# Kernel tuning notes

Hardware: AMD Instinct MI355X
Metric: run time of the kernel (lower is better)

## Reference

```python
import jax, jax.numpy as jnp
import numpy as np

B, S, L, F, CD, NH, E, HID = 4, 1024, 256, 512, 768, 8, 8, 2048


def _xavier(k, shape):
    std = float(np.sqrt(1.0 / (shape[-2] + shape[-1])))
    return jax.random.normal(k, shape, dtype=jnp.float32) * std


def setup_inputs() -> dict:
    key = jax.random.key(0)
    ks = iter(jax.random.split(key, 64))
    nk = lambda: next(ks)
    inp = {}
    inp['x_r'] = jax.random.normal(nk(), (B, S, F), jnp.float32)
    inp['x_i'] = jax.random.normal(nk(), (B, S, F), jnp.float32)
    inp['ctx_r'] = jax.random.normal(nk(), (B, L, CD), jnp.float32)
    inp['ctx_i'] = jax.random.normal(nk(), (B, L, CD), jnp.float32)
    inp['ln1_g'] = jnp.ones((F,), jnp.float32)
    inp['ln2_g'] = jnp.ones((F,), jnp.float32)
    inp['ln3_g'] = jnp.ones((F,), jnp.float32)
    for pref, shp in [('sa_q', (F, F)), ('sa_k', (F, F)), ('sa_v', (F, F)), ('sa_o', (F, F)),
                      ('ca_q', (F, F)), ('ca_k', (CD, F)), ('ca_v', (CD, F)), ('ca_o', (F, F))]:
        inp[pref + 'Wr'] = _xavier(nk(), shp)
        inp[pref + 'Wi'] = _xavier(nk(), shp)
        inp[pref + 'br'] = jnp.zeros((F,), jnp.float32)
        inp[pref + 'bi'] = jnp.zeros((F,), jnp.float32)
    inp['moe_W1r'] = _xavier(nk(), (E, F, HID))
    inp['moe_W1i'] = _xavier(nk(), (E, F, HID))
    inp['moe_b1r'] = jnp.zeros((E, HID), jnp.float32)
    inp['moe_b1i'] = jnp.zeros((E, HID), jnp.float32)
    inp['moe_mb'] = jnp.zeros((E, HID), jnp.float32)  # modReLU bias
    inp['moe_W2r'] = _xavier(nk(), (E, HID, F))
    inp['moe_W2i'] = _xavier(nk(), (E, HID, F))
    inp['moe_b2r'] = jnp.zeros((E, F), jnp.float32)
    inp['moe_b2i'] = jnp.zeros((E, F), jnp.float32)
    return inp


def _clin(xr, xi, Wr, Wi, br, bi):
    # (xr + i xi) @ (Wr + i Wi) + (br + i bi)
    return xr @ Wr - xi @ Wi + br, xr @ Wi + xi @ Wr + bi


def _cln(xr, xi, g, eps=1e-6):
    amp = jnp.sqrt(xr * xr + xi * xi + eps)
    s = g * (amp / (jnp.mean(amp, axis=-1, keepdims=True) + eps)) / (amp + eps)
    return xr * s, xi * s


def _modrelu(xr, xi, b, eps=1e-10):
    amp = jnp.sqrt(xr * xr + xi * xi + eps)
    s = jax.nn.relu(amp + b) / (amp + eps)
    return xr * s, xi * s


def _cattn(xr, xi, cr, ci, qWr, qWi, qbr, qbi, kWr, kWi, kbr, kbi,
           vWr, vWi, vbr, vbi, oWr, oWi, obr, obi, nh):
    qr, qi = _clin(xr, xi, qWr, qWi, qbr, qbi)
    kr, ki = _clin(cr, ci, kWr, kWi, kbr, kbi)
    vr, vi = _clin(cr, ci, vWr, vWi, vbr, vbi)
    Bt, Sq, Ft = qr.shape
    Sk = kr.shape[1]
    d = Ft // nh
    sp = lambda t: t.reshape(Bt, t.shape[1], nh, d).transpose(0, 2, 1, 3)  # b n s d
    Qr, Qi, Kr, Ki, Vr, Vi = sp(qr), sp(qi), sp(kr), sp(ki), sp(vr), sp(vi)
    scale = 1.0 / float(d) ** 0.5
    scores = (jnp.einsum('bnqd,bnkd->bnqk', Qr, Kr)
              + jnp.einsum('bnqd,bnkd->bnqk', Qi, Ki)) * scale
    w = jax.nn.softmax(scores, axis=-1)
    mix = lambda t: jnp.einsum('bnqk,bnkd->bnqd', w, t).transpose(0, 2, 1, 3).reshape(Bt, Sq, Ft)
    return _clin(mix(Vr), mix(Vi), oWr, oWi, obr, obi)


def reference(x_r, x_i, ctx_r, ctx_i, ln1_g, ln2_g, ln3_g,
              sa_qWr, sa_qWi, sa_qbr, sa_qbi, sa_kWr, sa_kWi, sa_kbr, sa_kbi,
              sa_vWr, sa_vWi, sa_vbr, sa_vbi, sa_oWr, sa_oWi, sa_obr, sa_obi,
              ca_qWr, ca_qWi, ca_qbr, ca_qbi, ca_kWr, ca_kWi, ca_kbr, ca_kbi,
              ca_vWr, ca_vWi, ca_vbr, ca_vbi, ca_oWr, ca_oWi, ca_obr, ca_obi,
              moe_W1r, moe_W1i, moe_b1r, moe_b1i, moe_mb,
              moe_W2r, moe_W2i, moe_b2r, moe_b2i):
    # self-attention block
    hr, hi = _cln(x_r, x_i, ln1_g)
    ar, ai = _cattn(hr, hi, hr, hi, sa_qWr, sa_qWi, sa_qbr, sa_qbi,
                    sa_kWr, sa_kWi, sa_kbr, sa_kbi, sa_vWr, sa_vWi, sa_vbr, sa_vbi,
                    sa_oWr, sa_oWi, sa_obr, sa_obi, NH)
    xr, xi = x_r + ar, x_i + ai
    # cross-attention block
    hr, hi = _cln(xr, xi, ln2_g)
    ar, ai = _cattn(hr, hi, ctx_r, ctx_i, ca_qWr, ca_qWi, ca_qbr, ca_qbi,
                    ca_kWr, ca_kWi, ca_kbr, ca_kbi, ca_vWr, ca_vWi, ca_vbr, ca_vbi,
                    ca_oWr, ca_oWi, ca_obr, ca_obi, NH)
    xr, xi = xr + ar, xi + ai
    # phase-routed MoE block
    hr, hi = _cln(xr, xi, ln3_g)
    phase = jnp.arctan2(hi, hr)
    token_phase = jnp.arctan2(jnp.mean(jnp.sin(phase), axis=-1),
                              jnp.mean(jnp.cos(phase), axis=-1))
    idx = jnp.clip(jnp.floor((token_phase + jnp.pi) / (2.0 * jnp.pi) * E).astype(jnp.int32), 0, E - 1)
    acc_r = jnp.zeros_like(hr)
    acc_i = jnp.zeros_like(hi)
    for e in range(E):  # dense-compute-then-mask, faithful to source
        ur, ui = _clin(hr, hi, moe_W1r[e], moe_W1i[e], moe_b1r[e], moe_b1i[e])
        ur, ui = _modrelu(ur, ui, moe_mb[e])
        yr, yi = _clin(ur, ui, moe_W2r[e], moe_W2i[e], moe_b2r[e], moe_b2i[e])
        m = (idx == e).astype(hr.dtype)[..., None]
        acc_r = acc_r + yr * m
        acc_i = acc_i + yi * m
    xr, xi = xr + acc_r, xi + acc_i
    return jnp.stack([xr, xi])  # [2, B, S, F] real/imag
```

## Files before the change

### kernel.cpp

```cpp
#include <hip/hip_runtime.h>
#include <hip/hip_bf16.h>
#include <math.h>


#define NTOK 4096
#define FF   512
#define CDIM 768
#define NEXP 8
#define HID  2048
#define TMAX 72
#define NPAD (TMAX * 64)

typedef __hip_bfloat16 bf16;
typedef short bf16x8 __attribute__((ext_vector_type(8)));
typedef float f32x4  __attribute__((ext_vector_type(4)));

struct Ptr6 { const float* p[6]; };

__device__ __forceinline__ short f2bf(float x) {
    unsigned u = __float_as_uint(x);
    unsigned r = (u + 0x7fff + ((u >> 16) & 1)) >> 16;
    return (short)r;
}
__device__ __forceinline__ float bf2f(short s) {
    return __uint_as_float(((unsigned)(unsigned short)s) << 16);
}
__device__ __forceinline__ void gload16(const void* g, void* l) {
    __builtin_amdgcn_global_load_lds(
        (const __attribute__((address_space(1))) unsigned int*)g,
        (__attribute__((address_space(3))) unsigned int*)l, 16, 0, 0);
}

__global__ __launch_bounds__(256)
void cln_kernel(const float* __restrict__ xr, const float* __restrict__ xi,
                const float* __restrict__ g,
                float* __restrict__ hr, float* __restrict__ hi)
{
    const int F = FF;
    long base = (long)blockIdx.x * F;
    int t = threadIdx.x;
    int j0 = t, j1 = t + 256;
    float xr0 = xr[base + j0], xi0 = xi[base + j0];
    float xr1 = xr[base + j1], xi1 = xi[base + j1];
    float a0 = sqrtf(xr0 * xr0 + xi0 * xi0 + 1e-6f);
    float a1 = sqrtf(xr1 * xr1 + xi1 * xi1 + 1e-6f);
    float s = a0 + a1;
#pragma unroll
    for (int off = 32; off >= 1; off >>= 1) s += __shfl_xor(s, off);
    __shared__ float wsum[4];
    if ((t & 63) == 0) wsum[t >> 6] = s;
    __syncthreads();
    float mean = (wsum[0] + wsum[1] + wsum[2] + wsum[3]) * (1.0f / 512.0f);
    float d0 = g[j0] * (a0 / (mean + 1e-6f)) / (a0 + 1e-6f);
    float d1 = g[j1] * (a1 / (mean + 1e-6f)) / (a1 + 1e-6f);
    hr[base + j0] = xr0 * d0;  hi[base + j0] = xi0 * d0;
    hr[base + j1] = xr1 * d1;  hi[base + j1] = xi1 * d1;
}

__global__ __launch_bounds__(256)
void expandA_x2(const float* __restrict__ sR, const float* __restrict__ sI,
                bf16* __restrict__ dR, bf16* __restrict__ dI, int K)
{
    int k = blockIdx.x * 256 + threadIdx.x;
    int m = blockIdx.y;
    long s = (long)m * K + k;
    long d = (long)m * 2 * K + k;
    float a = sR[s];
    bf16 ah = __float2bfloat16(a);
    dR[d] = ah; dR[d + K] = __float2bfloat16(a - __bfloat162float(ah));
    float b = sI[s];
    bf16 bh = __float2bfloat16(b);
    dI[d] = bh; dI[d + K] = __float2bfloat16(b - __bfloat162float(bh));
}

__global__ __launch_bounds__(256)
void convA_plain(const float* __restrict__ sR, const float* __restrict__ sI,
                 bf16* __restrict__ dR, bf16* __restrict__ dI, int K)
{
    int k = blockIdx.x * 256 + threadIdx.x;
    long s = (long)blockIdx.y * K + k;
    dR[s] = __float2bfloat16(sR[s]);
    dI[s] = __float2bfloat16(sI[s]);
}

__global__ __launch_bounds__(256)
void expandW_x2_packed(const float* __restrict__ sR, const float* __restrict__ sI,
                       bf16* __restrict__ dR, bf16* __restrict__ dI,
                       int N, int kdiv)
{
    int g = blockIdx.x * 256 + threadIdx.x;
    int nt = g >> 6, l = g & 63;
    int kc = blockIdx.y;
    int lo = (kc >= kdiv);
    int kb = (kc - (lo ? kdiv : 0)) * 32 + (l >> 4) * 8;
    int n  = nt * 16 + (l & 15);
    long dbase = ((long)kc * (N >> 4) + nt) * 512 + l * 8;
#pragma unroll
    for (int j = 0; j < 8; j++) {
        float a = sR[(long)(kb + j) * N + n];
        bf16 ah = __float2bfloat16(a);
        dR[dbase + j] = lo ? __float2bfloat16(a - __bfloat162float(ah)) : ah;
        float b = sI[(long)(kb + j) * N + n];
        bf16 bh = __float2bfloat16(b);
        dI[dbase + j] = lo ? __float2bfloat16(b - __bfloat162float(bh)) : bh;
    }
}

__global__ __launch_bounds__(256)
void convW_packed(const float* __restrict__ sR, const float* __restrict__ sI,
                  bf16* __restrict__ dR, bf16* __restrict__ dI,
                  int N, long estride)
{
    int g = blockIdx.x * 256 + threadIdx.x;
    int nt = g >> 6, l = g & 63;
    int kc = blockIdx.y;
    int e  = blockIdx.z;
    const float* srcR = sR + (long)e * estride;
    const float* srcI = sI + (long)e * estride;
    bf16* dstR = dR + (long)e * estride;
    bf16* dstI = dI + (long)e * estride;
    int kb = kc * 32 + (l >> 4) * 8;
    int n  = nt * 16 + (l & 15);
    long dbase = ((long)kc * (N >> 4) + nt) * 512 + l * 8;
#pragma unroll
    for (int j = 0; j < 8; j++) {
        dstR[dbase + j] = __float2bfloat16(srcR[(long)(kb + j) * N + n]);
        dstI[dbase + j] = __float2bfloat16(srcI[(long)(kb + j) * N + n]);
    }
}

template<bool X3, bool EXPERT, bool GATHER, bool MODRELU, bool RESID, bool OUTBF16>
__global__ __launch_bounds__(256)
void cgemm_mfma(const bf16* __restrict__ Ar, const bf16* __restrict__ Ai,
                int lda, int Kreal,
                const bf16* __restrict__ Wr0, const bf16* __restrict__ Wi0,
                long wz, long westride, int ntTot, int kdiv,
                Ptr6 bias, int bstride, const float* __restrict__ mb,
                const float* __restrict__ Rr, const float* __restrict__ Ri,
                void* __restrict__ Cr0, void* __restrict__ Ci0, long cz,
                int ldc, int Kp,
                const int* __restrict__ order, const int* __restrict__ tileExpert)
{
    __shared__ short sA[8192];
    __shared__ short sW[8192];
    int tm = blockIdx.x, tn = blockIdx.y, z = blockIdx.z;
    const bf16* Wr = Wr0 + (long)z * wz;
    const bf16* Wi = Wi0 + (long)z * wz;
    const float* br = bias.p[2 * z];
    const float* bi = bias.p[2 * z + 1];
    void* Crv = (char*)Cr0 + (long)z * cz;
    void* Civ = (char*)Ci0 + (long)z * cz;
    if (EXPERT) {
        int e = tileExpert[tm];
        if (e < 0) return;
        Wr += (long)e * westride;  Wi += (long)e * westride;
        br += (long)e * bstride;   bi += (long)e * bstride;
        if (MODRELU) mb += (long)e * bstride;
    }
    int t = threadIdx.x;
    int l = t & 63, jj = t >> 6;
    int riS = jj >> 1, kcS = jj & 1;
    const bf16* Asrc = riS ? Ai : Ar;
    const bf16* Wsrc = riS ? Wi : Wr;
    int kq8 = (l >> 4) * 8;
    long arb[4];
#pragma unroll
    for (int mt = 0; mt < 4; mt++) {
        int grow = tm * 64 + mt * 16 + (l & 15);
        int tok = grow;
        if (GATHER) { int gg = order[grow]; tok = (gg < 0) ? 0 : gg; }
        arb[mt] = (long)tok * lda;
    }
    int wm = jj & 1, wn = jj >> 1;

    f32x4 zf = {0.f, 0.f, 0.f, 0.f};
    f32x4 accR[2][2], accI[2][2];
#pragma unroll
    for (int a = 0; a < 2; a++)
#pragma unroll
        for (int b = 0; b < 2; b++) { accR[a][b] = zf; accI[a][b] = zf; }

// ... 70 lines not shown
}

__global__ __launch_bounds__(256)
void pack_kv(const float* __restrict__ kr, const float* __restrict__ ki,
             const float* __restrict__ vr, const float* __restrict__ vi,
             short* __restrict__ pK, short* __restrict__ pV, int Sk)
{
    const int F = FF;
    int kt = blockIdx.x, h = blockIdx.y, b = blockIdx.z;
    int nkt = gridDim.x;
    long blkbase = ((long)((b * 8 + h) * nkt) + kt) * 8192;
    int t = threadIdx.x;
#pragma unroll
    for (int it = 0; it < 2; it++) {
        int s = t + 256 * it;
        int sl = s & 63, g = s >> 6;
        int ri = g >> 2, c = (g >> 1) & 1, nt = g & 1;
        int sq = sl >> 4, sn = sl & 15;
        const float* src = ri ? ki : kr;
        long base = ((long)(b * Sk + kt * 32 + nt * 16 + sn)) * F + h * 64 + c * 32 + sq * 8;
        long outH = blkbase + ((((ri * 2 + 0) * 2 + c) * 2 + nt) * 64 + sl) * 8;
        long outL = blkbase + ((((ri * 2 + 1) * 2 + c) * 2 + nt) * 64 + sl) * 8;
#pragma unroll
        for (int j = 0; j < 8; j++) {
            float x = src[base + j];
            short xh = f2bf(x);
            pK[outH + j] = xh;
            pK[outL + j] = f2bf(x - bf2f(xh));
        }
    }
#pragma unroll
    for (int it = 0; it < 2; it++) {
        int s = t + 256 * it;
        int sl = s & 63, g = s >> 6;
        int ri = g >> 2, nt = g & 3;
        int sq = sl >> 4, sn = sl & 15;
        const float* src = ri ? vi : vr;
        long base = ((long)(b * Sk + kt * 32 + sq * 8)) * F + h * 64 + nt * 16 + sn;
        long outH = blkbase + (((ri * 2 + 0) * 4 + nt) * 64 + sl) * 8;
        long outL = blkbase + (((ri * 2 + 1) * 4 + nt) * 64 + sl) * 8;
#pragma unroll
        for (int j = 0; j < 8; j++) {
            float x = src[base + (long)j * F];
            short xh = f2bf(x);
            pV[outH + j] = xh;
            pV[outL + j] = f2bf(x - bf2f(xh));
        }
    }
}

__global__ __launch_bounds__(256)
void cattn_mfma(const float* __restrict__ qr, const float* __restrict__ qi,
                const short* __restrict__ pK, const short* __restrict__ pV,
                float* __restrict__ mr, float* __restrict__ mi,
                int S, int Sk)
{
    __shared__ short sK[8192];
    __shared__ short sV[8192];
    __shared__ short sP[5120];
    const int F = FF;
    int qt = blockIdx.x, h = blockIdx.y, b = blockIdx.z;
    int t = threadIdx.x;
    int w = t >> 6, l = t & 63, q = l >> 4, n16 = l & 15;

    bf16x8 qh_[2][2], ql_[2][2];
    {
        long qbase = ((long)(b * S + qt * 64 + w * 16 + n16)) * F + h * 64 + q * 8;
#pragma unroll
        for (int ri = 0; ri < 2; ri++) {
            const float* src = ri ? qi : qr;
#pragma unroll
            for (int c = 0; c < 2; c++) {
                float vv[8];
                *(float4*)&vv[0] = *(const float4*)&src[qbase + c * 32];
                *(float4*)&vv[4] = *(const float4*)&src[qbase + c * 32 + 4];
#pragma unroll
                for (int j = 0; j < 8; j++) {
                    short xh = f2bf(vv[j]);
                    qh_[ri][c][j] = xh;
                    ql_[ri][c][j] = f2bf(vv[j] - bf2f(xh));
                }
            }
        }
    }

    f32x4 zf = {0.f, 0.f, 0.f, 0.f};
    f32x4 oR[4], oI[4];
#pragma unroll
    for (int nt = 0; nt < 4; nt++) { oR[nt] = zf; oI[nt] = zf; }
    float m_run[4] = {-3.0e38f, -3.0e38f, -3.0e38f, -3.0e38f};
    float l_run[4] = {0.f, 0.f, 0.f, 0.f};

    int nkt = Sk >> 5;
    long pbh = (long)((b * 8 + h) * nkt) * 8192;
    for (int kt = 0; kt < nkt; kt++) {
        __syncthreads();
        long pb = pbh + (long)kt * 8192;
#pragma unroll
        for (int i = 0; i < 4; i++) {
            int bk = w * 4 + i;
            gload16(pK + pb + (bk << 9) + l * 8, &sK[bk << 9]);
            gload16(pV + pb + (bk << 9) + l * 8, &sV[bk << 9]);
        }
        __syncthreads();

        f32x4 sc[2];
        sc[0] = zf; sc[1] = zf;
// ... 19 lines not shown
            float s0 = sc[0][v] * 0.125f, s1 = sc[1][v] * 0.125f;
            float mx = fmaxf(s0, s1);
            mx = fmaxf(mx, __shfl_xor(mx, 1));
            mx = fmaxf(mx, __shfl_xor(mx, 2));
            mx = fmaxf(mx, __shfl_xor(mx, 4));
            mx = fmaxf(mx, __shfl_xor(mx, 8));
            float mnew = fmaxf(m_run[v], mx);
            float p0 = __expf(s0 - mnew), p1 = __expf(s1 - mnew);
            sc[0][v] = p0; sc[1][v] = p1;
            float ps = p0 + p1;
            ps += __shfl_xor(ps, 1);
            ps += __shfl_xor(ps, 2);
            ps += __shfl_xor(ps, 4);
            ps += __shfl_xor(ps, 8);
            alpha[v] = __expf(m_run[v] - mnew);
            l_run[v] = l_run[v] * alpha[v] + ps;
            m_run[v] = mnew;
        }
#pragma unroll
        for (int nt = 0; nt < 4; nt++)
#pragma unroll
            for (int v = 0; v < 4; v++) { oR[nt][v] *= alpha[v]; oI[nt][v] *= alpha[v]; }
        int pbase = w * 1280;
#pragma unroll
        for (int nt = 0; nt < 2; nt++)
#pragma unroll
            for (int v = 0; v < 4; v++) {
                float p = sc[nt][v];
                short ph = f2bf(p);
                short pl = f2bf(p - bf2f(ph));
                int idx = pbase + (q * 4 + v) * 40 + nt * 16 + n16;
                sP[idx] = ph;
                sP[idx + 640] = pl;
            }
        bf16x8 pH = *(const bf16x8*)&sP[pbase + n16 * 40 + q * 8];
        bf16x8 pL = *(const bf16x8*)&sP[pbase + 640 + n16 * 40 + q * 8];
#pragma unroll
        for (int nt = 0; nt < 4; nt++) {
            bf16x8 vh = *(const bf16x8*)&sV[(((0 * 2 + 0) * 4 + nt) * 64 + l) * 8];
            bf16x8 vl = *(const bf16x8*)&sV[(((0 * 2 + 1) * 4 + nt) * 64 + l) * 8];
            oR[nt] = __builtin_amdgcn_mfma_f32_16x16x32_bf16(pH, vh, oR[nt], 0, 0, 0);
            oR[nt] = __builtin_amdgcn_mfma_f32_16x16x32_bf16(pL, vh, oR[nt], 0, 0, 0);
            oR[nt] = __builtin_amdgcn_mfma_f32_16x16x32_bf16(pH, vl, oR[nt], 0, 0, 0);
            bf16x8 wh = *(const bf16x8*)&sV[(((1 * 2 + 0) * 4 + nt) * 64 + l) * 8];
            bf16x8 wl2 = *(const bf16x8*)&sV[(((1 * 2 + 1) * 4 + nt) * 64 + l) * 8];
            oI[nt] = __builtin_amdgcn_mfma_f32_16x16x32_bf16(pH, wh, oI[nt], 0, 0, 0);
            oI[nt] = __builtin_amdgcn_mfma_f32_16x16x32_bf16(pL, wh, oI[nt], 0, 0, 0);
            oI[nt] = __builtin_amdgcn_mfma_f32_16x16x32_bf16(pH, wl2, oI[nt], 0, 0, 0);
        }
    }
#pragma unroll
    for (int v = 0; v < 4; v++) {
        float inv = 1.0f / l_run[v];
        long obase = ((long)(b * S + qt * 64 + w * 16 + q * 4 + v)) * F + h * 64 + n16;
#pragma unroll
        for (int nt = 0; nt < 4; nt++) {
            mr[obase + nt * 16] = oR[nt][v] * inv;
            mi[obase + nt * 16] = oI[nt][v] * inv;
        }
    }
}

__global__ __launch_bounds__(256)
void route_kernel(const float* __restrict__ hr, const float* __restrict__ hi,
                  int* __restrict__ eidx)
{
    const int F = FF;
    long base = (long)blockIdx.x * F;
    int t = threadIdx.x;
    double ss = 0.0, cc = 0.0;
#pragma unroll
    for (int u = 0; u < 2; u++) {
        int j = t + u * 256;
        float ph = atan2f(hi[base + j], hr[base + j]);
        ss += (double)sinf(ph);
        cc += (double)cosf(ph);
    }
#pragma unroll
    for (int off = 32; off >= 1; off >>= 1) {
        ss += __shfl_xor(ss, off);
        cc += __shfl_xor(cc, off);
    }
    __shared__ double wss[4], wcc[4];
    if ((t & 63) == 0) { wss[t >> 6] = ss; wcc[t >> 6] = cc; }
    __syncthreads();
    if (t == 0) {
        float msin = (float)((wss[0] + wss[1] + wss[2] + wss[3]) * (1.0 / 512.0));
        float mcos = (float)((wcc[0] + wcc[1] + wcc[2] + wcc[3]) * (1.0 / 512.0));
        float tp = atan2f(msin, mcos);
        float a = (tp + 3.14159274101257324f) / 6.28318548202514648f * 8.0f;
        int k = (int)floorf(a);
        k = min(max(k, 0), NEXP - 1);
        eidx[blockIdx.x] = k;
    }
}

__global__ __launch_bounds__(256)
void moe_build_kernel(const int* __restrict__ eidx, int* __restrict__ order,
                      int* __restrict__ tileExpert)
{
    __shared__ int cnt[NEXP], segbase[NEXP], cursor[NEXP], tbase[NEXP];
    int t = threadIdx.x;
    if (t < NEXP) { cnt[t] = 0; cursor[t] = 0; }
    __syncthreads();
    for (int i = t; i < NTOK; i += 256) atomicAdd(&cnt[eidx[i]], 1);
    __syncthreads();
    if (t == 0) {
        int ob = 0, tb = 0;
        for (int e = 0; e < NEXP; e++) {
            segbase[e] = ob; tbase[e] = tb;
            int tiles = (cnt[e] + 63) >> 6;
            ob += tiles << 6; tb += tiles;
        }
    }
    __syncthreads();
    for (int i = t; i < NPAD; i += 256) order[i] = -1;
    if (t < TMAX) {
        int ex = -1;
        for (int e = 0; e < NEXP; e++) {
            int tiles = (cnt[e] + 63) >> 6;
            if (t >= tbase[e] && t < tbase[e] + tiles) ex = e;
        }
        tileExpert[t] = ex;
    }
    __syncthreads();
    for (int i = t; i < NTOK; i += 256) {
        int e = eidx[i];
        int pos = atomicAdd(&cursor[e], 1);
        order[segbase[e] + pos] = i;
    }
}

__global__ __launch_bounds__(256)
void combine_kernel(const int* __restrict__ order,
                    const float* __restrict__ xr, const float* __restrict__ xi,
                    const float* __restrict__ yr, const float* __restrict__ yi,
                    float* __restrict__ out)
{
    const int F = FF;
    int p = blockIdx.x;
    int tok = order[p];
    if (tok < 0) return;
    int t = threadIdx.x;
    float* outr = out;
    float* outi = out + (long)NTOK * FF;
#pragma unroll
    for (int u = 0; u < 2; u++) {
        int j = t + u * 256;
        long src = (long)p * F + j;
        long dst = (long)tok * F + j;
        outr[dst] = xr[dst] + yr[src];
        outi[dst] = xi[dst] + yi[src];
    }
}

extern "C" void kernel_launch(void* const* d_in, const int* in_sizes, int n_in,
                              void* d_out, int out_size, void* d_ws, size_t ws_size,
                              hipStream_t stream)
{
    (void)in_sizes; (void)n_in; (void)out_size; (void)ws_size;
    const float* x_r   = (const float*)d_in[0];
    const float* x_i   = (const float*)d_in[1];
    const float* ctx_r = (const float*)d_in[2];
    const float* ctx_i = (const float*)d_in[3];
    const float* ln1_g = (const float*)d_in[4];
    const float* ln2_g = (const float*)d_in[5];
    const float* ln3_g = (const float*)d_in[6];
    const float* sa_qWr = (const float*)d_in[7];   const float* sa_qWi = (const float*)d_in[8];
    const float* sa_qbr = (const float*)d_in[9];   const float* sa_qbi = (const float*)d_in[10];
    const float* sa_kWr = (const float*)d_in[11];  const float* sa_kWi = (const float*)d_in[12];
    const float* sa_kbr = (const float*)d_in[13];  const float* sa_kbi = (const float*)d_in[14];
    const float* sa_vWr = (const float*)d_in[15];  const float* sa_vWi = (const float*)d_in[16];
    const float* sa_vbr = (const float*)d_in[17];  const float* sa_vbi = (const float*)d_in[18];
    const float* sa_oWr = (const float*)d_in[19];  const float* sa_oWi = (const float*)d_in[20];
    const float* sa_obr = (const float*)d_in[21];  const float* sa_obi = (const float*)d_in[22];
    const float* ca_qWr = (const float*)d_in[23];  const float* ca_qWi = (const float*)d_in[24];
    const float* ca_qbr = (const float*)d_in[25];  const float* ca_qbi = (const float*)d_in[26];
    const float* ca_kWr = (const float*)d_in[27];  const float* ca_kWi = (const float*)d_in[28];
    const float* ca_kbr = (const float*)d_in[29];  const float* ca_kbi = (const float*)d_in[30];
    const float* ca_vWr = (const float*)d_in[31];  const float* ca_vWi = (const float*)d_in[32];
    const float* ca_vbr = (const float*)d_in[33];  const float* ca_vbi = (const float*)d_in[34];
    const float* ca_oWr = (const float*)d_in[35];  const float* ca_oWi = (const float*)d_in[36];
    const float* ca_obr = (const float*)d_in[37];  const float* ca_obi = (const float*)d_in[38];
    const float* moe_W1r = (const float*)d_in[39]; const float* moe_W1i = (const float*)d_in[40];
    const float* moe_b1r = (const float*)d_in[41]; const float* moe_b1i = (const float*)d_in[42];
    const float* moe_mb  = (const float*)d_in[43];
    const float* moe_W2r = (const float*)d_in[44]; const float* moe_W2i = (const float*)d_in[45];
    const float* moe_b2r = (const float*)d_in[46]; const float* moe_b2i = (const float*)d_in[47];
    float* out = (float*)d_out;

    char* W = (char*)d_ws;
    const long NF = (long)NTOK * FF;
    float* xr = (float*)(W + 0 * NF * 4);
    float* xi = (float*)(W + 1 * NF * 4);
    float* hr = (float*)(W + 2 * NF * 4);
    float* hi = (float*)(W + 3 * NF * 4);
    char* poolB = W + 4 * NF * 4;
    float* qr = (float*)poolB;                float* qi = (float*)(poolB + NF * 4);
    float* kr = (float*)(poolB + 2 * NF * 4); float* ki = (float*)(poolB + 3 * NF * 4);
    float* vr = (float*)(poolB + 4 * NF * 4); float* vi = (float*)(poolB + 5 * NF * 4);
    float* mr = (float*)(poolB + 6 * NF * 4); float* mi = (float*)(poolB + 7 * NF * 4);
    bf16* u_r = (bf16*)poolB;
    bf16* u_i = (bf16*)(poolB + 18874368);
    float* y_r = (float*)(poolB + 37748736);
    float* y_i = (float*)(poolB + 37748736 + 9437184);
    bf16* h3r = (bf16*)(poolB + 56623104);
    bf16* h3i = (bf16*)(poolB + 56623104 + 4194304);
    char* Q = W + 12 * NF * 4;
    bf16* A1r = (bf16*)Q;
    bf16* A1i = (bf16*)(Q + 8388608);
    bf16* A2r = (bf16*)(Q + 16777216);
    bf16* A2i = (bf16*)(Q + 19922944);
    char* WQ = Q + 23068672;
    const long PS1 = 524288;
    const long PS2 = 786432;
    bf16* saq_r = (bf16*)(WQ);                   bf16* saq_i = saq_r + PS1;
    bf16* sak_r = saq_r + 2 * PS1;               bf16* sak_i = saq_r + 3 * PS1;
    bf16* sav_r = saq_r + 4 * PS1;               bf16* sav_i = saq_r + 5 * PS1;
    bf16* sao_r = saq_r + 6 * PS1;               bf16* sao_i = saq_r + 7 * PS1;
    bf16* caq_r = saq_r + 8 * PS1;               bf16* caq_i = saq_r + 9 * PS1;
    bf16* cao_r = saq_r + 10 * PS1;              bf16* cao_i = saq_r + 11 * PS1;
    bf16* cak_r = saq_r + 12 * PS1;              bf16* cak_i = cak_r + PS2;
    bf16* cav_r = cak_r + 2 * PS2;               bf16* cav_i = cak_r + 3 * PS2;
    short* pKbuf = (short*)hr;
    short* pVbuf = (short*)Q;
    bf16* Wm_r = (bf16*)Q;
    bf16* Wm_i = (bf16*)(Q + 16777216);
    int* eidx       = (int*)(W + 12 * NF * 4 + 62914560);
    int* order      = eidx + NTOK;
    int* tileExpert = order + NPAD;

    dim3 blk(256);
    const long W1S = (long)FF * HID;
    const long CZ = 2 * NF * 4;
    Ptr6 bQKV = {{sa_qbr, sa_qbi, sa_kbr, sa_kbi, sa_vbr, sa_vbi}};
    Ptr6 bSAO = {{sa_obr, sa_obi, 0, 0, 0, 0}};
    Ptr6 bCAQ = {{ca_qbr, ca_qbi, 0, 0, 0, 0}};
    Ptr6 bCKV = {{ca_kbr, ca_kbi, ca_vbr, ca_vbi, 0, 0}};
    Ptr6 bCAO = {{ca_obr, ca_obi, 0, 0, 0, 0}};
    Ptr6 bM1  = {{moe_b1r, moe_b1i, 0, 0, 0, 0}};
    Ptr6 bM2  = {{moe_b2r, moe_b2i, 0, 0, 0, 0}};

    expandW_x2_packed<<<dim3(8, 32), blk, 0, stream>>>(sa_qWr, sa_qWi, saq_r, saq_i, FF, 16);
    expandW_x2_packed<<<dim3(8, 32), blk, 0, stream>>>(sa_kWr, sa_kWi, sak_r, sak_i, FF, 16);
    expandW_x2_packed<<<dim3(8, 32), blk, 0, stream>>>(sa_vWr, sa_vWi, sav_r, sav_i, FF, 16);
    expandW_x2_packed<<<dim3(8, 32), blk, 0, stream>>>(sa_oWr, sa_oWi, sao_r, sao_i, FF, 16);
    expandW_x2_packed<<<dim3(8, 32), blk, 0, stream>>>(ca_qWr, ca_qWi, caq_r, caq_i, FF, 16);
    expandW_x2_packed<<<dim3(8, 32), blk, 0, stream>>>(ca_oWr, ca_oWi, cao_r, cao_i, FF, 16);
    expandW_x2_packed<<<dim3(8, 48), blk, 0, stream>>>(ca_kWr, ca_kWi, cak_r, cak_i, FF, 24);
    expandW_x2_packed<<<dim3(8, 48), blk, 0, stream>>>(ca_vWr, ca_vWi, cav_r, cav_i, FF, 24);

    cln_kernel<<<NTOK, blk, 0, stream>>>(x_r, x_i, ln1_g, hr, hi);
    expandA_x2<<<dim3(2, NTOK), blk, 0, stream>>>(hr, hi, A1r, A1i, FF);
    cgemm_mfma<true,false,false,false,false,false><<<dim3(64, 8, 3), blk, 0, stream>>>(
        A1r, A1i, 1024, 512, saq_r, saq_i, 2 * PS1, 0, 32, 16,
        bQKV, 0, nullptr, nullptr, nullptr, qr, qi, CZ, FF, 1536, nullptr, nullptr);
    pack_kv<<<dim3(32, 8, 4), blk, 0, stream>>>(kr, ki, vr, vi, pKbuf, pVbuf, 1024);
    cattn_mfma<<<dim3(16, 8, 4), blk, 0, stream>>>(qr, qi, pKbuf, pVbuf, mr, mi, 1024, 1024);
    expandA_x2<<<dim3(2, NTOK), blk, 0, stream>>>(mr, mi, A1r, A1i, FF);
    cgemm_mfma<true,false,false,false,true,false><<<dim3(64, 8, 1), blk, 0, stream>>>(
        A1r, A1i, 1024, 512, sao_r, sao_i, 0, 0, 32, 16,
        bSAO, 0, nullptr, x_r, x_i, xr, xi, 0, FF, 1536, nullptr, nullptr);

    cln_kernel<<<NTOK, blk, 0, stream>>>(xr, xi, ln2_g, hr, hi);
    expandA_x2<<<dim3(2, NTOK), blk, 0, stream>>>(hr, hi, A1r, A1i, FF);
    cgemm_mfma<true,false,false,false,false,false><<<dim3(64, 8, 1), blk, 0, stream>>>(
        A1r, A1i, 1024, 512, caq_r, caq_i, 0, 0, 32, 16,
        bCAQ, 0, nullptr, nullptr, nullptr, qr, qi, 0, FF, 1536, nullptr, nullptr);
    expandA_x2<<<dim3(3, 1024), blk, 0, stream>>>(ctx_r, ctx_i, A2r, A2i, CDIM);
    cgemm_mfma<true,false,false,false,false,false><<<dim3(16, 8, 2), blk, 0, stream>>>(
        A2r, A2i, 1536, 768, cak_r, cak_i, 2 * PS2, 0, 32, 24,
        bCKV, 0, nullptr, nullptr, nullptr, kr, ki, CZ, FF, 2304, nullptr, nullptr);
    pack_kv<<<dim3(8, 8, 4), blk, 0, stream>>>(kr, ki, vr, vi, pKbuf, pVbuf, 256);
    cattn_mfma<<<dim3(16, 8, 4), blk, 0, stream>>>(qr, qi, pKbuf, pVbuf, mr, mi, 1024, 256);
    expandA_x2<<<dim3(2, NTOK), blk, 0, stream>>>(mr, mi, A1r, A1i, FF);
    cgemm_mfma<true,false,false,false,true,false><<<dim3(64, 8, 1), blk, 0, stream>>>(
        A1r, A1i, 1024, 512, cao_r, cao_i, 0, 0, 32, 16,
        bCAO, 0, nullptr, xr, xi, xr, xi, 0, FF, 1536, nullptr, nullptr);

    cln_kernel<<<NTOK, blk, 0, stream>>>(xr, xi, ln3_g, hr, hi);
    route_kernel<<<NTOK, blk, 0, stream>>>(hr, hi, eidx);
    moe_build_kernel<<<1, blk, 0, stream>>>(eidx, order, tileExpert);
    convA_plain<<<dim3(2, NTOK), blk, 0, stream>>>(hr, hi, h3r, h3i, FF);
    convW_packed<<<dim3(32, 16, 8), blk, 0, stream>>>(moe_W1r, moe_W1i, Wm_r, Wm_i, HID, W1S);
    cgemm_mfma<false,true,true,true,false,true><<<dim3(TMAX, 32, 1), blk, 0, stream>>>(
        h3r, h3i, 512, 512, Wm_r, Wm_i, 0, W1S, 128, 0,
        bM1, HID, moe_mb, nullptr, nullptr, u_r, u_i, 0, HID, 512, order, tileExpert);
    convW_packed<<<dim3(8, 64, 8), blk, 0, stream>>>(moe_W2r, moe_W2i, Wm_r, Wm_i, FF, W1S);
    cgemm_mfma<false,true,false,false,false,false><<<dim3(TMAX, 8, 1), blk, 0, stream>>>(
        u_r, u_i, 2048, 2048, Wm_r, Wm_i, 0, W1S, 32, 0,
        bM2, FF, nullptr, nullptr, nullptr, y_r, y_i, 0, FF, 2048, nullptr, tileExpert);
    combine_kernel<<<NPAD, blk, 0, stream>>>(order, xr, xi, y_r, y_i, out);
}
```

Measured before the change: 894.5 us.

## Fuse layernorm with bf16 split, routing, attention output; add 128x128 complex GEMM

Several ideas land together. The layernorm kernels now write the hi/lo bf16 split operands directly, and the third layernorm also computes the phase routing, which removes separate expand, convert and route kernels. Attention writes its output already split into bf16, and the eight weight-expansion launches are merged into one. A new 128x128-tile complex GEMM is used for the QKV projection and the first MoE layer, with expert segments padded to 128 rows. Larger tiles raise data reuse but cost LDS, registers and occupancy, and the coarser expert padding wastes more rows.

After: 866.5 us. -3.1%, faster.

```diff
diff --git a/kernel.cpp b/kernel.cpp
--- a/kernel.cpp
+++ b/kernel.cpp
@@ -8,14 +8,19 @@
 #define CDIM 768
 #define NEXP 8
 #define HID  2048
-#define TMAX 72
-#define NPAD (TMAX * 64)
+#define TMAX128 40
+#define NPAD128 (TMAX128 * 128)
 
 typedef __hip_bfloat16 bf16;
 typedef short bf16x8 __attribute__((ext_vector_type(8)));
 typedef float f32x4  __attribute__((ext_vector_type(4)));
 
 struct Ptr6 { const float* p[6]; };
+struct WPackAll {
+    const float* sR[8]; const float* sI[8];
+    bf16* dR[8]; bf16* dI[8];
+    int kdiv[8];
+};
 
 __device__ __forceinline__ short f2bf(float x) {
     unsigned u = __float_as_uint(x);
@@ -32,12 +37,11 @@
 }
 
 __global__ __launch_bounds__(256)
-void cln_kernel(const float* __restrict__ xr, const float* __restrict__ xi,
+void cln_expand(const float* __restrict__ xr, const float* __restrict__ xi,
                 const float* __restrict__ g,
-                float* __restrict__ hr, float* __restrict__ hi)
-{
-    const int F = FF;
-    long base = (long)blockIdx.x * F;
+                bf16* __restrict__ dR, bf16* __restrict__ dI)
+{
+    long base = (long)blockIdx.x * FF;
     int t = threadIdx.x;
     int j0 = t, j1 = t + 256;
     float xr0 = xr[base + j0], xi0 = xi[base + j0];
@@ -53,8 +57,66 @@
     float mean = (wsum[0] + wsum[1] + wsum[2] + wsum[3]) * (1.0f / 512.0f);
     float d0 = g[j0] * (a0 / (mean + 1e-6f)) / (a0 + 1e-6f);
     float d1 = g[j1] * (a1 / (mean + 1e-6f)) / (a1 + 1e-6f);
-    hr[base + j0] = xr0 * d0;  hi[base + j0] = xi0 * d0;
-    hr[base + j1] = xr1 * d1;  hi[base + j1] = xi1 * d1;
+    long d = (long)blockIdx.x * 1024;
+    float h; bf16 hh;
+    h = xr0 * d0; hh = __float2bfloat16(h);
+    dR[d + j0] = hh; dR[d + 512 + j0] = __float2bfloat16(h - __bfloat162float(hh));
+    h = xi0 * d0; hh = __float2bfloat16(h);
+    dI[d + j0] = hh; dI[d + 512 + j0] = __float2bfloat16(h - __bfloat162float(hh));
+    h = xr1 * d1; hh = __float2bfloat16(h);
+    dR[d + j1] = hh; dR[d + 512 + j1] = __float2bfloat16(h - __bfloat162float(hh));
+    h = xi1 * d1; hh = __float2bfloat16(h);
+    dI[d + j1] = hh; dI[d + 512 + j1] = __float2bfloat16(h - __bfloat162float(hh));
+}
+
+__global__ __launch_bounds__(256)
+void cln_route(const float* __restrict__ xr, const float* __restrict__ xi,
+               const float* __restrict__ g,
+               bf16* __restrict__ h3r, bf16* __restrict__ h3i,
+               int* __restrict__ eidx)
+{
+    long base = (long)blockIdx.x * FF;
+    int t = threadIdx.x;
+    int j0 = t, j1 = t + 256;
+    float xr0 = xr[base + j0], xi0 = xi[base + j0];
+    float xr1 = xr[base + j1], xi1 = xi[base + j1];
+    float a0 = sqrtf(xr0 * xr0 + xi0 * xi0 + 1e-6f);
+    float a1 = sqrtf(xr1 * xr1 + xi1 * xi1 + 1e-6f);
+    float s = a0 + a1;
+#pragma unroll
+    for (int off = 32; off >= 1; off >>= 1) s += __shfl_xor(s, off);
+    __shared__ float wsum[4];
+    __shared__ double wss[4], wcc[4];
+    if ((t & 63) == 0) wsum[t >> 6] = s;
+    __syncthreads();
+    float mean = (wsum[0] + wsum[1] + wsum[2] + wsum[3]) * (1.0f / 512.0f);
+    float d0 = g[j0] * (a0 / (mean + 1e-6f)) / (a0 + 1e-6f);
+    float d1 = g[j1] * (a1 / (mean + 1e-6f)) / (a1 + 1e-6f);
+    float h0r = xr0 * d0, h0i = xi0 * d0;
+    float h1r = xr1 * d1, h1i = xi1 * d1;
+    h3r[base + j0] = __float2bfloat16(h0r);
+    h3i[base + j0] = __float2bfloat16(h0i);
+    h3r[base + j1] = __float2bfloat16(h1r);
+    h3i[base + j1] = __float2bfloat16(h1i);
+    float ph0 = atan2f(h0i, h0r), ph1 = atan2f(h1i, h1r);
+    double ss = (double)sinf(ph0) + (double)sinf(ph1);
+    double cc = (double)cosf(ph0) + (double)cosf(ph1);
+#pragma unroll
+    for (int off = 32; off >= 1; off >>= 1) {
+        ss += __shfl_xor(ss, off);
+        cc += __shfl_xor(cc, off);
+    }
+    if ((t & 63) == 0) { wss[t >> 6] = ss; wcc[t >> 6] = cc; }
+    __syncthreads();
+    if (t == 0) {
+        float msin = (float)((wss[0] + wss[1] + wss[2] + wss[3]) * (1.0 / 512.0));
+        float mcos = (float)((wcc[0] + wcc[1] + wcc[2] + wcc[3]) * (1.0 / 512.0));
+        float tp = atan2f(msin, mcos);
+        float a = (tp + 3.14159274101257324f) / 6.28318548202514648f * 8.0f;
+        int k = (int)floorf(a);
+        k = min(max(k, 0), NEXP - 1);
+        eidx[blockIdx.x] = k;
+    }
 }
 
 __global__ __launch_bounds__(256)
@@ -74,27 +136,21 @@
 }
 
 __global__ __launch_bounds__(256)
-void convA_plain(const float* __restrict__ sR, const float* __restrict__ sI,
-                 bf16* __restrict__ dR, bf16* __restrict__ dI, int K)
-{
-    int k = blockIdx.x * 256 + threadIdx.x;
-    long s = (long)blockIdx.y * K + k;
-    dR[s] = __float2bfloat16(sR[s]);
-    dI[s] = __float2bfloat16(sI[s]);
-}
-
-__global__ __launch_bounds__(256)
-void expandW_x2_packed(const float* __restrict__ sR, const float* __restrict__ sI,
-                       bf16* __restrict__ dR, bf16* __restrict__ dI,
-                       int N, int kdiv)
-{
+void expandW_all(WPackAll p)
+{
+    int z = blockIdx.z;
+    int kdiv = p.kdiv[z];
+    int kc = blockIdx.y;
+    if (kc >= 2 * kdiv) return;
+    const int N = FF;
     int g = blockIdx.x * 256 + threadIdx.x;
     int nt = g >> 6, l = g & 63;
-    int kc = blockIdx.y;
     int lo = (kc >= kdiv);
     int kb = (kc - (lo ? kdiv : 0)) * 32 + (l >> 4) * 8;
     int n  = nt * 16 + (l & 15);
     long dbase = ((long)kc * (N >> 4) + nt) * 512 + l * 8;
+    const float* sR = p.sR[z]; const float* sI = p.sI[z];
+    bf16* dR = p.dR[z]; bf16* dI = p.dI[z];
 #pragma unroll
     for (int j = 0; j < 8; j++) {
         float a = sR[(long)(kb + j) * N + n];
@@ -127,6 +183,128 @@
         dstR[dbase + j] = __float2bfloat16(srcR[(long)(kb + j) * N + n]);
         dstI[dbase + j] = __float2bfloat16(srcI[(long)(kb + j) * N + n]);
     }
+}
+
+template<bool X3, bool EXPERT, bool GATHER, bool MODRELU, bool OUTBF16>
+__global__ __launch_bounds__(256, 2)
+void cgemm128(const bf16* __restrict__ Ar, const bf16* __restrict__ Ai,
+              int lda, int Kreal,
+              const bf16* __restrict__ Wr0, const bf16* __restrict__ Wi0,
+              long wz, long westride, int ntTot, int kdiv,
+              Ptr6 bias, int bstride, const float* __restrict__ mb,
+              void* __restrict__ Cr0, void* __restrict__ Ci0, long cz,
+              int ldc, int Kp,
+              const int* __restrict__ order, const int* __restrict__ tileExpert)
+{
+    __shared__ short sA[16384];
+    __shared__ short sW[16384];
+    int tm = blockIdx.x, tn = blockIdx.y, z = blockIdx.z;
+    const bf16* Wr = Wr0 + (long)z * wz;
+    const bf16* Wi = Wi0 + (long)z * wz;
+    const float* br = bias.p[2 * z];
+    const float* bi = bias.p[2 * z + 1];
+    void* Crv = (char*)Cr0 + (long)z * cz;
+    void* Civ = (char*)Ci0 + (long)z * cz;
+    if (EXPERT) {
+        int e = tileExpert[tm];
+        if (e < 0) return;
+        Wr += (long)e * westride;  Wi += (long)e * westride;
+        br += (long)e * bstride;   bi += (long)e * bstride;
+        if (MODRELU) mb += (long)e * bstride;
+    }
+    int t = threadIdx.x;
+    int l = t & 63, w = t >> 6;
+    int riS = w >> 1, kcS = w & 1;
+    const bf16* Asrc = riS ? Ai : Ar;
+    const bf16* Wsrc = riS ? Wi : Wr;
+    int kq8 = (l >> 4) * 8;
+    long arb[8];
+#pragma unroll
+    for (int mt = 0; mt < 8; mt++) {
+        int grow = tm * 128 + mt * 16 + (l & 15);
+        int tok = grow;
+        if (GATHER) { int gg = order[grow]; tok = (gg < 0) ? 0 : gg; }
+        arb[mt] = (long)tok * lda;
+    }
+    int wm = w & 1, wn = w >> 1;
+
+    f32x4 zf = {0.f, 0.f, 0.f, 0.f};
+    f32x4 accR[4][4], accI[4][4];
+#pragma unroll
+    for (int a = 0; a < 4; a++)
+#pragma unroll
+        for (int b = 0; b < 4; b++) { accR[a][b] = zf; accI[a][b] = zf; }
+
+    const bf16x8 sgn = {(short)0x8000,(short)0x8000,(short)0x8000,(short)0x8000,
+                        (short)0x8000,(short)0x8000,(short)0x8000,(short)0x8000};
+
+    for (int k0 = 0; k0 < Kp; k0 += 64) {
+        __syncthreads();
+        int lc = k0 + kcS * 32;
+        int acol = (X3 && lc >= 2 * Kreal) ? lc - 2 * Kreal : lc;
+#pragma unroll
+        for (int mt = 0; mt < 8; mt++)
+            gload16(Asrc + arb[mt] + acol + kq8,
+                    &sA[(((riS * 2 + kcS) * 8 + mt) << 9)]);
+        int kcl = (k0 >> 5) + kcS;
+        int pkc = (X3 && kcl >= kdiv) ? kcl - kdiv : kcl;
+        const bf16* wb = Wsrc + (((long)pkc * ntTot + tn * 8) << 9) + l * 8;
+#pragma unroll
+        for (int ntl = 0; ntl < 8; ntl++)
+            gload16(wb + (ntl << 9),
+                    &sW[(((riS * 2 + kcS) * 8 + ntl) << 9)]);
+        __syncthreads();
+#pragma unroll
+        for (int kc = 0; kc < 2; kc++) {
+            bf16x8 wrf[4], wif[4];
+#pragma unroll
+            for (int sn = 0; sn < 4; sn++) {
+                wrf[sn] = *(const bf16x8*)&sW[(((kc * 8) + wn * 4 + sn) << 9) + l * 8];
+                wif[sn] = *(const bf16x8*)&sW[((((2 + kc) * 8) + wn * 4 + sn) << 9) + l * 8];
+            }
+#pragma unroll
+            for (int sm = 0; sm < 4; sm++) {
+                bf16x8 ar = *(const bf16x8*)&sA[(((kc * 8) + wm * 4 + sm) << 9) + l * 8];
+                bf16x8 ai = *(const bf16x8*)&sA[((((2 + kc) * 8) + wm * 4 + sm) << 9) + l * 8];
+                bf16x8 na = ai ^ sgn;
+#pragma unroll
+                for (int sn = 0; sn < 4; sn++) {
+                    accR[sm][sn] = __builtin_amdgcn_mfma_f32_16x16x32_bf16(ar, wrf[sn], accR[sm][sn], 0, 0, 0);
+                    accR[sm][sn] = __builtin_amdgcn_mfma_f32_16x16x32_bf16(na, wif[sn], accR[sm][sn], 0, 0, 0);
+                    accI[sm][sn] = __builtin_amdgcn_mfma_f32_16x16x32_bf16(ar, wif[sn], accI[sm][sn], 0, 0, 0);
+                    accI[sm][sn] = __builtin_amdgcn_mfma_f32_16x16x32_bf16(ai, wrf[sn], accI[sm][sn], 0, 0, 0);
+                }
+            }
+        }
+    }
+#pragma unroll
+    for (int sm = 0; sm < 4; sm++)
+#pragma unroll
+        for (int sn = 0; sn < 4; sn++) {
+            int row0 = tm * 128 + wm * 64 + sm * 16 + (l >> 4) * 4;
+            int col  = tn * 128 + wn * 64 + sn * 16 + (l & 15);
+            float bre = br[col], bie = bi[col];
+            float mbe = MODRELU ? mb[col] : 0.f;
+#pragma unroll
+            for (int v = 0; v < 4; v++) {
+                int row = row0 + v;
+                float vr = accR[sm][sn][v] + bre;
+                float vi = accI[sm][sn][v] + bie;
+                if (MODRELU) {
+                    float amp = sqrtf(vr * vr + vi * vi + 1e-10f);
+                    float sc = fmaxf(amp + mbe, 0.f) / (amp + 1e-10f);
+                    vr *= sc; vi *= sc;
+                }
+                long cidx = (long)row * ldc + col;
+                if (OUTBF16) {
+                    ((bf16*)Crv)[cidx] = __float2bfloat16(vr);
+                    ((bf16*)Civ)[cidx] = __float2bfloat16(vi);
+                } else {
+                    ((float*)Crv)[cidx] = vr;
+                    ((float*)Civ)[cidx] = vi;
+                }
+            }
+        }
 }
 
 template<bool X3, bool EXPERT, bool GATHER, bool MODRELU, bool RESID, bool OUTBF16>
@@ -303,7 +481,7 @@
 __global__ __launch_bounds__(256)
 void cattn_mfma(const float* __restrict__ qr, const float* __restrict__ qi,
                 const short* __restrict__ pK, const short* __restrict__ pV,
-                float* __restrict__ mr, float* __restrict__ mi,
+                bf16* __restrict__ dR, bf16* __restrict__ dI,
                 int S, int Sk)
 {
     __shared__ short sK[8192];
@@ -429,54 +607,27 @@
 #pragma unroll
     for (int v = 0; v < 4; v++) {
         float inv = 1.0f / l_run[v];
-        long obase = ((long)(b * S + qt * 64 + w * 16 + q * 4 + v)) * F + h * 64 + n16;
+        long rbase = ((long)(b * S + qt * 64 + w * 16 + q * 4 + v)) * 1024;
 #pragma unroll
         for (int nt = 0; nt < 4; nt++) {
-            mr[obase + nt * 16] = oR[nt][v] * inv;
-            mi[obase + nt * 16] = oI[nt][v] * inv;
-        }
-    }
-}
-
-__global__ __launch_bounds__(256)
-void route_kernel(const float* __restrict__ hr, const float* __restrict__ hi,
-                  int* __restrict__ eidx)
-{
-    const int F = FF;
-    long base = (long)blockIdx.x * F;
-    int t = threadIdx.x;
-    double ss = 0.0, cc = 0.0;
-#pragma unroll
-    for (int u = 0; u < 2; u++) {
-        int j = t + u * 256;
-        float ph = atan2f(hi[base + j], hr[base + j]);
-        ss += (double)sinf(ph);
-        cc += (double)cosf(ph);
-    }
-#pragma unroll
-    for (int off = 32; off >= 1; off >>= 1) {
-        ss += __shfl_xor(ss, off);
-        cc += __shfl_xor(cc, off);
-    }
-    __shared__ double wss[4], wcc[4];
-    if ((t & 63) == 0) { wss[t >> 6] = ss; wcc[t >> 6] = cc; }
-    __syncthreads();
-    if (t == 0) {
-        float msin = (float)((wss[0] + wss[1] + wss[2] + wss[3]) * (1.0 / 512.0));
-        float mcos = (float)((wcc[0] + wcc[1] + wcc[2] + wcc[3]) * (1.0 / 512.0));
-        float tp = atan2f(msin, mcos);
-        float a = (tp + 3.14159274101257324f) / 6.28318548202514648f * 8.0f;
-        int k = (int)floorf(a);
-        k = min(max(k, 0), NEXP - 1);
-        eidx[blockIdx.x] = k;
+            int col = h * 64 + nt * 16 + n16;
+            float vr = oR[nt][v] * inv;
+            bf16 hh = __float2bfloat16(vr);
+            dR[rbase + col] = hh;
+            dR[rbase + 512 + col] = __float2bfloat16(vr - __bfloat162float(hh));
+            float vi = oI[nt][v] * inv;
+            bf16 hi2 = __float2bfloat16(vi);
+            dI[rbase + col] = hi2;
+            dI[rbase + 512 + col] = __float2bfloat16(vi - __bfloat162float(hi2));
+        }
     }
 }
 
 __global__ __launch_bounds__(256)
 void moe_build_kernel(const int* __restrict__ eidx, int* __restrict__ order,
-                      int* __restrict__ tileExpert)
-{
-    __shared__ int cnt[NEXP], segbase[NEXP], cursor[NEXP], tbase[NEXP];
+                      int* __restrict__ te128, int* __restrict__ te64)
+{
+    __shared__ int cnt[NEXP], segbase[NEXP], cursor[NEXP], tb128[NEXP], n128[NEXP];
     int t = threadIdx.x;
     if (t < NEXP) { cnt[t] = 0; cursor[t] = 0; }
     __syncthreads();
@@ -485,20 +636,26 @@
     if (t == 0) {
         int ob = 0, tb = 0;
         for (int e = 0; e < NEXP; e++) {
-            segbase[e] = ob; tbase[e] = tb;
-            int tiles = (cnt[e] + 63) >> 6;
-            ob += tiles << 6; tb += tiles;
+            segbase[e] = ob; tb128[e] = tb;
+            int tiles = (cnt[e] + 127) >> 7;
+            n128[e] = tiles;
+            ob += tiles << 7; tb += tiles;
         }
     }
     __syncthreads();
-    for (int i = t; i < NPAD; i += 256) order[i] = -1;
-    if (t < TMAX) {
+    for (int i = t; i < NPAD128; i += 256) order[i] = -1;
+    if (t < TMAX128) {
         int ex = -1;
-        for (int e = 0; e < NEXP; e++) {
-            int tiles = (cnt[e] + 63) >> 6;
-            if (t >= tbase[e] && t < tbase[e] + tiles) ex = e;
-        }
-        tileExpert[t] = ex;
+        for (int e = 0; e < NEXP; e++)
+            if (t >= tb128[e] && t < tb128[e] + n128[e]) ex = e;
+        te128[t] = ex;
+    }
+    if (t >= 64 && t < 64 + 2 * TMAX128) {
+        int tt = t - 64;
+        int ex = -1;
+        for (int e = 0; e < NEXP; e++)
+            if (tt >= tb128[e] * 2 && tt < (tb128[e] + n128[e]) * 2) ex = e;
+        te64[tt] = ex;
     }
     __syncthreads();
     for (int i = t; i < NTOK; i += 256) {
@@ -568,22 +725,23 @@
 
     char* W = (char*)d_ws;
     const long NF = (long)NTOK * FF;
-    float* xr = (float*)(W + 0 * NF * 4);
-    float* xi = (float*)(W + 1 * NF * 4);
-    float* hr = (float*)(W + 2 * NF * 4);
-    float* hi = (float*)(W + 3 * NF * 4);
-    char* poolB = W + 4 * NF * 4;
-    float* qr = (float*)poolB;                float* qi = (float*)(poolB + NF * 4);
-    float* kr = (float*)(poolB + 2 * NF * 4); float* ki = (float*)(poolB + 3 * NF * 4);
-    float* vr = (float*)(poolB + 4 * NF * 4); float* vi = (float*)(poolB + 5 * NF * 4);
-    float* mr = (float*)(poolB + 6 * NF * 4); float* mi = (float*)(poolB + 7 * NF * 4);
+    const long NF4 = NF * 4;
+    float* xr = (float*)(W + 0 * NF4);
+    float* xi = (float*)(W + 1 * NF4);
+    char* base2 = W + 2 * NF4;
+    short* pKbuf = (short*)base2;
+    bf16* h3r = (bf16*)base2;
+    bf16* h3i = (bf16*)(base2 + 4194304);
+    char* poolB = W + 4 * NF4;
+    float* qr = (float*)poolB;                float* qi = (float*)(poolB + NF4);
+    float* kr = (float*)(poolB + 2 * NF4);    float* ki = (float*)(poolB + 3 * NF4);
+    float* vr = (float*)(poolB + 4 * NF4);    float* vi = (float*)(poolB + 5 * NF4);
+    short* pVbuf = (short*)(poolB + 6 * NF4);
     bf16* u_r = (bf16*)poolB;
-    bf16* u_i = (bf16*)(poolB + 18874368);
-    float* y_r = (float*)(poolB + 37748736);
-    float* y_i = (float*)(poolB + 37748736 + 9437184);
-    bf16* h3r = (bf16*)(poolB + 56623104);
-    bf16* h3i = (bf16*)(poolB + 56623104 + 4194304);
-    char* Q = W + 12 * NF * 4;
+    bf16* u_i = (bf16*)(poolB + 20971520);
+    float* y_r = (float*)(poolB + 41943040);
+    float* y_i = (float*)(poolB + 52428800);
+    char* Q = W + 12 * NF4;
     bf16* A1r = (bf16*)Q;
     bf16* A1i = (bf16*)(Q + 8388608);
     bf16* A2r = (bf16*)(Q + 16777216);
@@ -599,17 +757,17 @@
     bf16* cao_r = saq_r + 10 * PS1;              bf16* cao_i = saq_r + 11 * PS1;
     bf16* cak_r = saq_r + 12 * PS1;              bf16* cak_i = cak_r + PS2;
     bf16* cav_r = cak_r + 2 * PS2;               bf16* cav_i = cak_r + 3 * PS2;
-    short* pKbuf = (short*)hr;
-    short* pVbuf = (short*)Q;
     bf16* Wm_r = (bf16*)Q;
     bf16* Wm_i = (bf16*)(Q + 16777216);
-    int* eidx       = (int*)(W + 12 * NF * 4 + 62914560);
-    int* order      = eidx + NTOK;
-    int* tileExpert = order + NPAD;
+    char* ints = W + 12 * NF4 + 41943040 + 524288;
+    int* eidx  = (int*)ints;
+    int* order = eidx + NTOK;
+    int* te128 = order + NPAD128;
+    int* te64  = te128 + 64;
 
     dim3 blk(256);
     const long W1S = (long)FF * HID;
-    const long CZ = 2 * NF * 4;
+    const long CZ = 2 * NF4;
     Ptr6 bQKV = {{sa_qbr, sa_qbi, sa_kbr, sa_kbi, sa_vbr, sa_vbi}};
     Ptr6 bSAO = {{sa_obr, sa_obi, 0, 0, 0, 0}};
     Ptr6 bCAQ = {{ca_qbr, ca_qbi, 0, 0, 0, 0}};
@@ -618,29 +776,28 @@
     Ptr6 bM1  = {{moe_b1r, moe_b1i, 0, 0, 0, 0}};
     Ptr6 bM2  = {{moe_b2r, moe_b2i, 0, 0, 0, 0}};
 
-    expandW_x2_packed<<<dim3(8, 32), blk, 0, stream>>>(sa_qWr, sa_qWi, saq_r, saq_i, FF, 16);
-    expandW_x2_packed<<<dim3(8, 32), blk, 0, stream>>>(sa_kWr, sa_kWi, sak_r, sak_i, FF, 16);
-    expandW_x2_packed<<<dim3(8, 32), blk, 0, stream>>>(sa_vWr, sa_vWi, sav_r, sav_i, FF, 16);
-    expandW_x2_packed<<<dim3(8, 32), blk, 0, stream>>>(sa_oWr, sa_oWi, sao_r, sao_i, FF, 16);
-    expandW_x2_packed<<<dim3(8, 32), blk, 0, stream>>>(ca_qWr, ca_qWi, caq_r, caq_i, FF, 16);
-    expandW_x2_packed<<<dim3(8, 32), blk, 0, stream>>>(ca_oWr, ca_oWi, cao_r, cao_i, FF, 16);
-    expandW_x2_packed<<<dim3(8, 48), blk, 0, stream>>>(ca_kWr, ca_kWi, cak_r, cak_i, FF, 24);
-    expandW_x2_packed<<<dim3(8, 48), blk, 0, stream>>>(ca_vWr, ca_vWi, cav_r, cav_i, FF, 24);
-
-    cln_kernel<<<NTOK, blk, 0, stream>>>(x_r, x_i, ln1_g, hr, hi);
-    expandA_x2<<<dim3(2, NTOK), blk, 0, stream>>>(hr, hi, A1r, A1i, FF);
-    cgemm_mfma<true,false,false,false,false,false><<<dim3(64, 8, 3), blk, 0, stream>>>(
+    WPackAll wp;
+    wp.sR[0]=sa_qWr; wp.sI[0]=sa_qWi; wp.dR[0]=saq_r; wp.dI[0]=saq_i; wp.kdiv[0]=16;
+    wp.sR[1]=sa_kWr; wp.sI[1]=sa_kWi; wp.dR[1]=sak_r; wp.dI[1]=sak_i; wp.kdiv[1]=16;
+    wp.sR[2]=sa_vWr; wp.sI[2]=sa_vWi; wp.dR[2]=sav_r; wp.dI[2]=sav_i; wp.kdiv[2]=16;
+    wp.sR[3]=sa_oWr; wp.sI[3]=sa_oWi; wp.dR[3]=sao_r; wp.dI[3]=sao_i; wp.kdiv[3]=16;
+    wp.sR[4]=ca_qWr; wp.sI[4]=ca_qWi; wp.dR[4]=caq_r; wp.dI[4]=caq_i; wp.kdiv[4]=16;
+    wp.sR[5]=ca_oWr; wp.sI[5]=ca_oWi; wp.dR[5]=cao_r; wp.dI[5]=cao_i; wp.kdiv[5]=16;
+    wp.sR[6]=ca_kWr; wp.sI[6]=ca_kWi; wp.dR[6]=cak_r; wp.dI[6]=cak_i; wp.kdiv[6]=24;
+    wp.sR[7]=ca_vWr; wp.sI[7]=ca_vWi; wp.dR[7]=cav_r; wp.dI[7]=cav_i; wp.kdiv[7]=24;
+    expandW_all<<<dim3(8, 48, 8), blk, 0, stream>>>(wp);
+
+    cln_expand<<<NTOK, blk, 0, stream>>>(x_r, x_i, ln1_g, A1r, A1i);
+    cgemm128<true,false,false,false,false><<<dim3(32, 4, 3), blk, 0, stream>>>(
         A1r, A1i, 1024, 512, saq_r, saq_i, 2 * PS1, 0, 32, 16,
-        bQKV, 0, nullptr, nullptr, nullptr, qr, qi, CZ, FF, 1536, nullptr, nullptr);
+        bQKV, 0, nullptr, qr, qi, CZ, FF, 1536, nullptr, nullptr);
     pack_kv<<<dim3(32, 8, 4), blk, 0, stream>>>(kr, ki, vr, vi, pKbuf, pVbuf, 1024);
-    cattn_mfma<<<dim3(16, 8, 4), blk, 0, stream>>>(qr, qi, pKbuf, pVbuf, mr, mi, 1024, 1024);
-    expandA_x2<<<dim3(2, NTOK), blk, 0, stream>>>(mr, mi, A1r, A1i, FF);
+    cattn_mfma<<<dim3(16, 8, 4), blk, 0, stream>>>(qr, qi, pKbuf, pVbuf, A1r, A1i, 1024, 1024);
     cgemm_mfma<true,false,false,false,true,false><<<dim3(64, 8, 1), blk, 0, stream>>>(
         A1r, A1i, 1024, 512, sao_r, sao_i, 0, 0, 32, 16,
         bSAO, 0, nullptr, x_r, x_i, xr, xi, 0, FF, 1536, nullptr, nullptr);
 
-    cln_kernel<<<NTOK, blk, 0, stream>>>(xr, xi, ln2_g, hr, hi);
-    expandA_x2<<<dim3(2, NTOK), blk, 0, stream>>>(hr, hi, A1r, A1i, FF);
+    cln_expand<<<NTOK, blk, 0, stream>>>(xr, xi, ln2_g, A1r, A1i);
     cgemm_mfma<true,false,false,false,false,false><<<dim3(64, 8, 1), blk, 0, stream>>>(
         A1r, A1i, 1024, 512, caq_r, caq_i, 0, 0, 32, 16,
         bCAQ, 0, nullptr, nullptr, nullptr, qr, qi, 0, FF, 1536, nullptr, nullptr);
@@ -649,23 +806,20 @@
         A2r, A2i, 1536, 768, cak_r, cak_i, 2 * PS2, 0, 32, 24,
         bCKV, 0, nullptr, nullptr, nullptr, kr, ki, CZ, FF, 2304, nullptr, nullptr);
     pack_kv<<<dim3(8, 8, 4), blk, 0, stream>>>(kr, ki, vr, vi, pKbuf, pVbuf, 256);
-    cattn_mfma<<<dim3(16, 8, 4), blk, 0, stream>>>(qr, qi, pKbuf, pVbuf, mr, mi, 1024, 256);
-    expandA_x2<<<dim3(2, NTOK), blk, 0, stream>>>(mr, mi, A1r, A1i, FF);
+    cattn_mfma<<<dim3(16, 8, 4), blk, 0, stream>>>(qr, qi, pKbuf, pVbuf, A1r, A1i, 1024, 256);
     cgemm_mfma<true,false,false,false,true,false><<<dim3(64, 8, 1), blk, 0, stream>>>(
         A1r, A1i, 1024, 512, cao_r, cao_i, 0, 0, 32, 16,
         bCAO, 0, nullptr, xr, xi, xr, xi, 0, FF, 1536, nullptr, nullptr);
 
-    cln_kernel<<<NTOK, blk, 0, stream>>>(xr, xi, ln3_g, hr, hi);
-    route_kernel<<<NTOK, blk, 0, stream>>>(hr, hi, eidx);
-    moe_build_kernel<<<1, blk, 0, stream>>>(eidx, order, tileExpert);
-    convA_plain<<<dim3(2, NTOK), blk, 0, stream>>>(hr, hi, h3r, h3i, FF);
+    cln_route<<<NTOK, blk, 0, stream>>>(xr, xi, ln3_g, h3r, h3i, eidx);
+    moe_build_kernel<<<1, blk, 0, stream>>>(eidx, order, te128, te64);
     convW_packed<<<dim3(32, 16, 8), blk, 0, stream>>>(moe_W1r, moe_W1i, Wm_r, Wm_i, HID, W1S);
-    cgemm_mfma<false,true,true,true,false,true><<<dim3(TMAX, 32, 1), blk, 0, stream>>>(
+    cgemm128<false,true,true,true,true><<<dim3(TMAX128, 16, 1), blk, 0, stream>>>(
         h3r, h3i, 512, 512, Wm_r, Wm_i, 0, W1S, 128, 0,
-        bM1, HID, moe_mb, nullptr, nullptr, u_r, u_i, 0, HID, 512, order, tileExpert);
+        bM1, HID, moe_mb, u_r, u_i, 0, HID, 512, order, te128);
     convW_packed<<<dim3(8, 64, 8), blk, 0, stream>>>(moe_W2r, moe_W2i, Wm_r, Wm_i, FF, W1S);
-    cgemm_mfma<false,true,false,false,false,false><<<dim3(TMAX, 8, 1), blk, 0, stream>>>(
+    cgemm_mfma<false,true,false,false,false,false><<<dim3(2 * TMAX128, 8, 1), blk, 0, stream>>>(
         u_r, u_i, 2048, 2048, Wm_r, Wm_i, 0, W1S, 32, 0,
-        bM2, FF, nullptr, nullptr, nullptr, y_r, y_i, 0, FF, 2048, nullptr, tileExpert);
-    combine_kernel<<<NPAD, blk, 0, stream>>>(order, xr, xi, y_r, y_i, out);
-}
+        bM2, FF, nullptr, nullptr, nullptr, y_r, y_i, 0, FF, 2048, nullptr, te64);
+    combine_kernel<<<NPAD128, blk, 0, stream>>>(order, xr, xi, y_r, y_i, out);
+}
```
